# Performance work log

Measured on AMD Instinct MI355X. Metric: run time of the kernel, lower is better.

## Reference

```python
import jax, jax.numpy as jnp
import numpy as np

B, T, D = 32, 4096, 768
HEADS, DK, DV = 4, 64, 64
REL_W = 32
HIDDEN = 256


def setup_inputs() -> dict:
    key = jax.random.key(0)
    ks = jax.random.split(key, 12)
    H_sent = jax.random.normal(ks[0], (B, T, D), dtype=jnp.float32)
    # realistic padding: each sample has a random valid length in [2048, T]
    lengths = jax.random.randint(ks[1], (B,), 2048, T + 1)
    attention_mask_sent = (jnp.arange(T)[None, :] < lengths[:, None]).astype(jnp.int32)
    noun_pos = jax.random.randint(ks[2], (B,), 0, 2048).astype(jnp.int32)
    pooled_fields = jax.random.normal(ks[3], (B, D), dtype=jnp.float32)
    # xavier-uniform for (heads, d, dk): fan_in=d, fan_out=dk per torch semantics
    def xavier(k, shape, fan_in, fan_out):
        lim = float(np.sqrt(6.0 / (fan_in + fan_out)))
        return jax.random.uniform(k, shape, jnp.float32, -lim, lim)
    WQ = xavier(ks[4], (HEADS, D, DK), D, DK)
    WK = xavier(ks[5], (HEADS, D, DK), D, DK)
    WV = xavier(ks[6], (HEADS, D, DV), D, DV)
    rel_bias = jnp.zeros((HEADS, 2 * REL_W + 1), jnp.float32) + 0.01 * jax.random.normal(ks[7], (HEADS, 2 * REL_W + 1))
    in_proj = D + HEADS * DV + D  # 1792
    proj_w = xavier(ks[8], (HIDDEN, in_proj), in_proj, HIDDEN)
    proj_b = jnp.zeros((HIDDEN,), jnp.float32)
    mlp_w = xavier(ks[9], (2, HIDDEN), HIDDEN, 2)
    mlp_b = jnp.zeros((2,), jnp.float32)
    return {
        "H_sent": H_sent, "attention_mask_sent": attention_mask_sent,
        "noun_pos": noun_pos, "pooled_fields": pooled_fields,
        "WQ": WQ, "WK": WK, "WV": WV, "rel_bias": rel_bias,
        "proj_w": proj_w, "proj_b": proj_b, "mlp_w": mlp_w, "mlp_b": mlp_b,
    }


def reference(H_sent, attention_mask_sent, noun_pos, pooled_fields,
              WQ, WK, WV, rel_bias, proj_w, proj_b, mlp_w, mlp_b):
    b, t, d = H_sent.shape
    heads, _, dk = WQ.shape
    w = (rel_bias.shape[1] - 1) // 2
    # gather single query vector per sample
    h_i = H_sent[jnp.arange(b), noun_pos]  # (B, d)
    Q = jnp.einsum('bd,hdk->bhk', h_i, WQ)        # (B, H, dk)
    K = jnp.einsum('btd,hdk->bthk', H_sent, WK)   # (B, T, H, dk)
    V = jnp.einsum('btd,hdv->bthv', H_sent, WV)   # (B, T, H, dv)
    scores = jnp.einsum('bhk,bthk->bht', Q, K) / jnp.sqrt(jnp.float32(dk))  # (B,H,T)
    # relative-position bias gathered by clamped delta
    delta = jnp.clip(jnp.arange(t)[None, :] - noun_pos[:, None], -w, w) + w  # (B,T)
    rb = rel_bias[:, delta]                        # (H, B, T)
    scores = scores + jnp.transpose(rb, (1, 0, 2))
    scores = jnp.where(attention_mask_sent[:, None, :] == 0, jnp.float32(-1e9), scores)
    alpha = jax.nn.softmax(scores, axis=-1)        # (B, H, T)
    c = jnp.einsum('bht,bthv->bhv', alpha, V).reshape(b, -1)  # (B, H*dv)
    r = jnp.concatenate([h_i, c, pooled_fields], axis=-1)     # (B, d + H*dv + d)
    hdn = jax.nn.gelu(r @ proj_w.T + proj_b, approximate=False)
    logits = hdn @ mlp_w.T + mlp_b                 # (B, 2)
    return logits
```

## Files before the change

### kernel.cpp

```cpp
#include <hip/hip_runtime.h>
#include <math.h>

#define BB 32
#define TT 4096
#define DD 768
#define NH 4
#define RELW 32
#define NREL 65
#define HIDDEN 256
#define INPROJ 1792

#define NCH 32
#define CROWS (TT / NCH)
#define TROWS 8
#define C4 (DD / 4)

#define WAITVM6() asm volatile("s_waitcnt vmcnt(6)" ::: "memory")
#define WAITVM0() asm volatile("s_waitcnt vmcnt(0)" ::: "memory")

__device__ __forceinline__ void gl_lds16(const float* g, float* l) {
    __builtin_amdgcn_global_load_lds(
        (const __attribute__((address_space(1))) float*)(uintptr_t)g,
        (__attribute__((address_space(3))) float*)(uintptr_t)l,
        16, 0, 0);
}

template <int CTRL, int RMASK>
__device__ __forceinline__ float upd0(float x) {
    return __int_as_float(__builtin_amdgcn_update_dpp(
        0, __float_as_int(x), CTRL, RMASK, 0xf, true));
}
__device__ __forceinline__ float wave_sum64(float x) {
    x += upd0<0x111, 0xf>(x);
    x += upd0<0x112, 0xf>(x);
    x += upd0<0x114, 0xf>(x);
    x += upd0<0x118, 0xf>(x);
    x += upd0<0x142, 0xa>(x);
    x += upd0<0x143, 0xc>(x);
    return __int_as_float(__builtin_amdgcn_readlane(__float_as_int(x), 63));
}

__global__ __launch_bounds__(256) void kA(const float* __restrict__ H,
                                          const int* __restrict__ noun_pos,
                                          const float* __restrict__ WQ,
                                          const float* __restrict__ WK,
                                          float* __restrict__ R,
                                          float* __restrict__ qk_ws) {
    int b = blockIdx.x / NH, h = blockIdx.x % NH;
    __shared__ float hi_s[DD];
    __shared__ float q_s[64];
    int tn = noun_pos[b];
    const float* Hrow = H + ((size_t)b * TT + tn) * DD;
    for (int d = threadIdx.x; d < DD; d += 256) {
        float v = Hrow[d];
        hi_s[d] = v;
        if (h == 0) R[(size_t)b * INPROJ + d] = v;
    }
    __syncthreads();
    if (threadIdx.x < 64) {
        int k = threadIdx.x;
        const float* wq = WQ + (size_t)h * DD * 64 + k;
        float acc = 0.f;
        for (int d = 0; d < DD; ++d) acc += hi_s[d] * wq[(size_t)d * 64];
        q_s[k] = acc;
    }
    __syncthreads();
    for (int d = threadIdx.x; d < DD; d += 256) {
        const float* wk = WK + ((size_t)h * DD + d) * 64;
        float acc = 0.f;
        #pragma unroll
        for (int k = 0; k < 64; ++k) acc += q_s[k] * wk[k];
        qk_ws[((size_t)b * NH + h) * DD + d] = acc * 0.125f;
    }
}

#define DOT(ACC, CV, QV) ACC += CV.x*QV.x + CV.y*QV.y + CV.z*QV.z + CV.w*QV.w

#define HUPD(M, L, S0, S1, B0, B1, B2)                                    \
  {                                                                        \
    float nm = fmaxf(M, fmaxf(S0, S1));                                    \
    if (nm > M + 8.0f) {                                                   \
      float sc = __expf(M - nm);                                           \
      L *= sc;                                                             \
      B0.x*=sc; B0.y*=sc; B0.z*=sc; B0.w*=sc;                              \
      B1.x*=sc; B1.y*=sc; B1.z*=sc; B1.w*=sc;                              \
      B2.x*=sc; B2.y*=sc; B2.z*=sc; B2.w*=sc;                              \
      M = nm;                                                              \
    }                                                                      \
    float p0 = __expf(S0 - M), p1 = __expf(S1 - M);                        \
    L += p0 + p1;                                                          \
    B0.x += p0*c0.x + p1*c3.x; B0.y += p0*c0.y + p1*c3.y;                  \
    B0.z += p0*c0.z + p1*c3.z; B0.w += p0*c0.w + p1*c3.w;                  \
    B1.x += p0*c1.x + p1*c4.x; B1.y += p0*c1.y + p1*c4.y;                  \
    B1.z += p0*c1.z + p1*c4.z; B1.w += p0*c1.w + p1*c4.w;                  \
    B2.x += p0*c2.x + p1*c5.x; B2.y += p0*c2.y + p1*c5.y;                  \
    B2.z += p0*c2.z + p1*c5.z; B2.w += p0*c2.w + p1*c5.w;                  \
  }

__global__ __launch_bounds__(256, 3) void kFlash(const float* __restrict__ H,
                                                 const int* __restrict__ mask,
                                                 const int* __restrict__ noun_pos,
                                                 const float* __restrict__ rel_bias,
                                                 const float* __restrict__ qk_ws,
                                                 float* __restrict__ macc,
                                                 float* __restrict__ ml) {
    const int b   = blockIdx.x / NCH;
    const int ch  = blockIdx.x % NCH;
    const int tid = threadIdx.x;
    const int wave = tid >> 6, lane = tid & 63;

    __shared__ float4 Hts[2][TROWS * C4];
    __shared__ float4 rbL[CROWS];
    __shared__ float mls[4][8];
    __shared__ int snl;

    const int t0 = ch * CROWS;
    const int tn = noun_pos[b];

    if (tid == 0) snl = 0;
    __syncthreads();
    if (tid < CROWS) {
        int t = t0 + tid;
        int dl = t - tn; dl = dl < -RELW ? -RELW : (dl > RELW ? RELW : dl);
        int mm = mask[(size_t)b * TT + t];
        float4 rv;
        if (mm) {
            rv.x = rel_bias[0 * NREL + dl + RELW];
            rv.y = rel_bias[1 * NREL + dl + RELW];
            rv.z = rel_bias[2 * NREL + dl + RELW];
            rv.w = rel_bias[3 * NREL + dl + RELW];
            atomicMax(&snl, tid + 1);
        } else {
            rv.x = rv.y = rv.z = rv.w = -2.0e9f;
        }
        rbL[tid] = rv;
    }

    float4 qr[NH][3];
    {
        const float4* qk4 = (const float4*)(qk_ws + (size_t)b * NH * DD);
        #pragma unroll
        for (int h = 0; h < NH; ++h)
            #pragma unroll
            for (int j = 0; j < 3; ++j)
                qr[h][j] = qk4[h * C4 + j * 64 + lane];
    }

    __syncthreads();
    const int NTE = (snl + TROWS - 1) / TROWS;

    if (NTE == 0) {
        float4 z = {0.f, 0.f, 0.f, 0.f};
        float4* mo = (float4*)(macc + (size_t)blockIdx.x * NH * DD);
        int h = tid >> 6, ln = tid & 63;
        #pragma unroll
        for (int j = 0; j < 3; ++j) mo[h * C4 + j * 64 + ln] = z;
        if (tid < NH) {
            float* mp = ml + (size_t)blockIdx.x * NH * 2;
            mp[tid * 2 + 0] = -3.0e38f; mp[tid * 2 + 1] = 0.f;
        }
        return;
    }

    float m0 = -3.0e38f, m1 = -3.0e38f, m2 = -3.0e38f, m3 = -3.0e38f;
    float l0 = 0.f, l1 = 0.f, l2 = 0.f, l3 = 0.f;
    float4 A00{0,0,0,0}, A01{0,0,0,0}, A02{0,0,0,0};
    float4 A10{0,0,0,0}, A11{0,0,0,0}, A12{0,0,0,0};
    float4 A20{0,0,0,0}, A21{0,0,0,0}, A22{0,0,0,0};
    float4 A30{0,0,0,0}, A31{0,0,0,0}, A32{0,0,0,0};

    const float* Hc = H + ((size_t)b * TT + t0) * DD;
    const int woff = wave * 1536;

    {
        float* dst = (float*)&Hts[0][0] + woff;
        const float* src = Hc + woff;
        #pragma unroll
        for (int i = 0; i < 6; ++i)
            gl_lds16(src + i * 256 + lane * 4, dst + i * 256);
    }

    #pragma unroll 1
    for (int t = 0; t < NTE; ++t) {
        const int cur = t & 1;
        if (t + 1 < NTE) {
            float* dst = (float*)&Hts[cur ^ 1][0] + woff;
            const float* src = Hc + (size_t)(t + 1) * TROWS * DD + woff;
            #pragma unroll
            for (int i = 0; i < 6; ++i)
                gl_lds16(src + i * 256 + lane * 4, dst + i * 256);
            WAITVM6();
        } else {
            WAITVM0();
        }
        const float4* Hr = &Hts[cur][0] + wave * 384;
        float4 c0 = Hr[lane],       c1 = Hr[64 + lane],  c2 = Hr[128 + lane];
        float4 c3 = Hr[192 + lane], c4 = Hr[256 + lane], c5 = Hr[320 + lane];

        float s00 = 0, s01 = 0, s02 = 0, s03 = 0;
        float s10 = 0, s11 = 0, s12 = 0, s13 = 0;
        DOT(s00, c0, qr[0][0]); DOT(s00, c1, qr[0][1]); DOT(s00, c2, qr[0][2]);
        DOT(s01, c0, qr[1][0]); DOT(s01, c1, qr[1][1]); DOT(s01, c2, qr[1][2]);
        DOT(s02, c0, qr[2][0]); DOT(s02, c1, qr[2][1]); DOT(s02, c2, qr[2][2]);
        DOT(s03, c0, qr[3][0]); DOT(s03, c1, qr[3][1]); DOT(s03, c2, qr[3][2]);
        DOT(s10, c3, qr[0][0]); DOT(s10, c4, qr[0][1]); DOT(s10, c5, qr[0][2]);
        DOT(s11, c3, qr[1][0]); DOT(s11, c4, qr[1][1]); DOT(s11, c5, qr[1][2]);
        DOT(s12, c3, qr[2][0]); DOT(s12, c4, qr[2][1]); DOT(s12, c5, qr[2][2]);
        DOT(s13, c3, qr[3][0]); DOT(s13, c4, qr[3][1]); DOT(s13, c5, qr[3][2]);
        float r00 = wave_sum64(s00), r01 = wave_sum64(s01);
        float r02 = wave_sum64(s02), r03 = wave_sum64(s03);
        float r10 = wave_sum64(s10), r11 = wave_sum64(s11);
        float r12 = wave_sum64(s12), r13 = wave_sum64(s13);
        float4 rb0 = rbL[t * TROWS + 2 * wave];
        float4 rb1 = rbL[t * TROWS + 2 * wave + 1];
        r00 += rb0.x; r01 += rb0.y; r02 += rb0.z; r03 += rb0.w;
        r10 += rb1.x; r11 += rb1.y; r12 += rb1.z; r13 += rb1.w;
        HUPD(m0, l0, r00, r10, A00, A01, A02);
        HUPD(m1, l1, r01, r11, A10, A11, A12);
        HUPD(m2, l2, r02, r12, A20, A21, A22);
        HUPD(m3, l3, r03, r13, A30, A31, A32);
    }

    __syncthreads();
    float4* scr = &Hts[0][0];
    #pragma unroll
    for (int j = 0; j < 3; ++j) {
        scr[(wave * 4 + 0) * C4 + j * 64 + lane] = j == 0 ? A00 : (j == 1 ? A01 : A02);
        scr[(wave * 4 + 1) * C4 + j * 64 + lane] = j == 0 ? A10 : (j == 1 ? A11 : A12);
        scr[(wave * 4 + 2) * C4 + j * 64 + lane] = j == 0 ? A20 : (j == 1 ? A21 : A22);
        scr[(wave * 4 + 3) * C4 + j * 64 + lane] = j == 0 ? A30 : (j == 1 ? A31 : A32);
    }
    if (lane == 0) {
        mls[wave][0] = m0; mls[wave][1] = l0; mls[wave][2] = m1; mls[wave][3] = l1;
        mls[wave][4] = m2; mls[wave][5] = l2; mls[wave][6] = m3; mls[wave][7] = l3;
    }
    __syncthreads();
    {
        int h = tid >> 6, ln = tid & 63;
        float M = fmaxf(fmaxf(mls[0][h*2], mls[1][h*2]), fmaxf(mls[2][h*2], mls[3][h*2]));
        float w0 = __expf(mls[0][h*2] - M), w1 = __expf(mls[1][h*2] - M);
        float w2 = __expf(mls[2][h*2] - M), w3 = __expf(mls[3][h*2] - M);
        float4* mo = (float4*)(macc + (size_t)blockIdx.x * NH * DD);
        #pragma unroll
        for (int j = 0; j < 3; ++j) {
            float4 v0 = scr[(0*4 + h) * C4 + j * 64 + ln];
            float4 v1 = scr[(1*4 + h) * C4 + j * 64 + ln];
            float4 v2 = scr[(2*4 + h) * C4 + j * 64 + ln];
            float4 v3 = scr[(3*4 + h) * C4 + j * 64 + ln];
            float4 v;
            v.x = w0*v0.x + w1*v1.x + w2*v2.x + w3*v3.x;
            v.y = w0*v0.y + w1*v1.y + w2*v2.y + w3*v3.y;
            v.z = w0*v0.z + w1*v1.z + w2*v2.z + w3*v3.z;
            v.w = w0*v0.w + w1*v1.w + w2*v2.w + w3*v3.w;
            mo[h * C4 + j * 64 + ln] = v;
        }
        if (tid < NH) {
            int hh = tid;
            float Mh = fmaxf(fmaxf(mls[0][hh*2], mls[1][hh*2]), fmaxf(mls[2][hh*2], mls[3][hh*2]));
            float Lh = __expf(mls[0][hh*2] - Mh) * mls[0][hh*2+1]
                     + __expf(mls[1][hh*2] - Mh) * mls[1][hh*2+1]
                     + __expf(mls[2][hh*2] - Mh) * mls[2][hh*2+1]
                     + __expf(mls[3][hh*2] - Mh) * mls[3][hh*2+1];
            float* mp = ml + (size_t)blockIdx.x * NH * 2;
            mp[hh * 2 + 0] = Mh; mp[hh * 2 + 1] = Lh;
        }
    }
}

__global__ __launch_bounds__(256) void kT(const float* __restrict__ pw,
                                          float* __restrict__ pwT) {
    int o = blockIdx.x * 256 + threadIdx.x;
    int j = o / INPROJ, i = o % INPROJ;
    pwT[(size_t)i * HIDDEN + j] = pw[o];
}

__global__ __launch_bounds__(256) void kComb(const float* __restrict__ macc,
                                             const float* __restrict__ ml,
                                             float* __restrict__ hbar) {
    int blk = blockIdx.x;
    int b = blk / 12, rem = blk % 12, h = rem / 3, dseg = rem % 3;
    int d = dseg * 256 + threadIdx.x;
    const float* mlb = ml + (size_t)b * NCH * 8 + h * 2;
    float M = -3.0e38f;
    #pragma unroll 8
    for (int c = 0; c < NCH; ++c) M = fmaxf(M, mlb[(size_t)c * 8]);
    float L = 0.f;
    #pragma unroll 8
    for (int c = 0; c < NCH; ++c)
        L += __expf(mlb[(size_t)c * 8] - M) * mlb[(size_t)c * 8 + 1];
    float acc = 0.f;
    const float* mc = macc + ((size_t)b * NCH * NH + h) * DD + d;
    #pragma unroll 8
    for (int c = 0; c < NCH; ++c)
        acc += __expf(mlb[(size_t)c * 8] - M) * mc[(size_t)c * NH * DD];
    hbar[((size_t)b * NH + h) * DD + d] = acc / L;
}

__global__ __launch_bounds__(256) void kC2(const float* __restrict__ hbar,
                                           const float* __restrict__ WV,
                                           const float* __restrict__ pooled,
                                           float* __restrict__ R) {
    int b = blockIdx.x;
    int h = threadIdx.x >> 6, v = threadIdx.x & 63;
    const float* hb = hbar + ((size_t)b * NH + h) * DD;
    const float* wv = WV + (size_t)h * DD * 64 + v;
    float acc = 0.f;
    #pragma unroll 8
    for (int d = 0; d < DD; ++d) acc += hb[d] * wv[(size_t)d * 64];
    R[(size_t)b * INPROJ + DD + threadIdx.x] = acc;
    for (int i = threadIdx.x; i < DD; i += 256)
        R[(size_t)b * INPROJ + DD + 256 + i] = pooled[(size_t)b * DD + i];
}

__global__ __launch_bounds__(256) void kH1(const float* __restrict__ R,
                                           const float* __restrict__ pwT,
                                           float* __restrict__ part2) {
    int b = blockIdx.x / 7, seg = blockIdx.x % 7;
    int j = threadIdx.x;
    __shared__ float r_s[256];
    r_s[j] = R[(size_t)b * INPROJ + seg * 256 + j];
    __syncthreads();
    float acc = 0.f;
    const float* pT = pwT + (size_t)seg * 256 * HIDDEN + j;
    #pragma unroll 8
    for (int i = 0; i < 256; ++i) acc += r_s[i] * pT[(size_t)i * HIDDEN];
    part2[((size_t)b * 7 + seg) * HIDDEN + j] = acc;
}

__global__ __launch_bounds__(256) void kH2(const float* __restrict__ part2,
                                           const float* __restrict__ pb,
                                           const float* __restrict__ mw,
                                           const float* __restrict__ mb,
                                           float* __restrict__ out) {
    int b = blockIdx.x, j = threadIdx.x;
    float acc = pb[j];
    #pragma unroll
    for (int s = 0; s < 7; ++s) acc += part2[((size_t)b * 7 + s) * HIDDEN + j];
    float hdn = 0.5f * acc * (1.f + erff(acc * 0.70710678118654752f));
    float p0 = hdn * mw[j];
    float p1 = hdn * mw[HIDDEN + j];
    #pragma unroll
    for (int off = 32; off; off >>= 1) {
        p0 += __shfl_xor(p0, off);
        p1 += __shfl_xor(p1, off);
    }
    __shared__ float r0[4], r1[4];
    if ((j & 63) == 0) {
        r0[j >> 6] = p0;
        r1[j >> 6] = p1;
    }
    __syncthreads();
    if (j == 0) {
        out[b * 2 + 0] = r0[0] + r0[1] + r0[2] + r0[3] + mb[0];
        out[b * 2 + 1] = r1[0] + r1[1] + r1[2] + r1[3] + mb[1];
    }
}

extern "C" void kernel_launch(void* const* d_in, const int* in_sizes, int n_in,
                              void* d_out, int out_size, void* d_ws, size_t ws_size,
                              hipStream_t stream) {
    const float* H      = (const float*)d_in[0];
    const int*   mask   = (const int*)d_in[1];
    const int*   noun   = (const int*)d_in[2];
    const float* pooled = (const float*)d_in[3];
    const float* WQ     = (const float*)d_in[4];
    const float* WK     = (const float*)d_in[5];
    const float* WV     = (const float*)d_in[6];
    const float* relb   = (const float*)d_in[7];
    const float* pw     = (const float*)d_in[8];
    const float* pb     = (const float*)d_in[9];
    const float* mw     = (const float*)d_in[10];
    const float* mb     = (const float*)d_in[11];
    float* out = (float*)d_out;

    float* ws    = (float*)d_ws;
    float* R     = ws;
    float* qk    = R + (size_t)BB * INPROJ;
    float* macc  = qk + (size_t)BB * NH * DD;
    float* ml    = macc + (size_t)BB * NCH * NH * DD;
    float* hbar  = ml + (size_t)BB * NCH * NH * 2;
    float* pwT   = hbar + (size_t)BB * NH * DD;
    float* part2 = pwT + (size_t)INPROJ * HIDDEN;

    kA<<<BB * NH, 256, 0, stream>>>(H, noun, WQ, WK, R, qk);
    kT<<<(HIDDEN * INPROJ) / 256, 256, 0, stream>>>(pw, pwT);
    kFlash<<<BB * NCH, 256, 0, stream>>>(H, mask, noun, relb, qk, macc, ml);
    kComb<<<BB * 12, 256, 0, stream>>>(macc, ml, hbar);
    kC2<<<BB, 256, 0, stream>>>(hbar, WV, pooled, R);
    kH1<<<BB * 7, 256, 0, stream>>>(R, pwT, part2);
    kH2<<<BB, 256, 0, stream>>>(part2, pb, mw, mb, out);
}
```

Before: 152.6 us.

## Fuse split-softmax combine with V projection and merge head MLP kernels

Merges the chunk-combine and value-projection kernels into one per-(batch, head) block that keeps the combined hidden vector in shared memory, and folds the two head-MLP kernels into one block per sample that runs the full 1792-long dot product. The pooled-field copy moves into the first kernel, and the Q projection there is spread across all 256 threads with a shared-memory partial reduction. The goal is fewer launches and fewer global round trips for intermediates. In exchange the head kernel runs only 32 blocks with a long serial loop, which may lower parallelism.

Result: no change. 154.3 us (+1.1%).

```diff
diff --git a/kernel.cpp b/kernel.cpp
--- a/kernel.cpp
+++ b/kernel.cpp
@@ -44,10 +44,12 @@
                                           const int* __restrict__ noun_pos,
                                           const float* __restrict__ WQ,
                                           const float* __restrict__ WK,
+                                          const float* __restrict__ pooled,
                                           float* __restrict__ R,
                                           float* __restrict__ qk_ws) {
     int b = blockIdx.x / NH, h = blockIdx.x % NH;
     __shared__ float hi_s[DD];
+    __shared__ float qpart[4][64];
     __shared__ float q_s[64];
     int tn = noun_pos[b];
     const float* Hrow = H + ((size_t)b * TT + tn) * DD;
@@ -55,15 +57,21 @@
         float v = Hrow[d];
         hi_s[d] = v;
         if (h == 0) R[(size_t)b * INPROJ + d] = v;
-    }
-    __syncthreads();
-    if (threadIdx.x < 64) {
-        int k = threadIdx.x;
+        if (h == 1) R[(size_t)b * INPROJ + DD + NH * 64 + d] = pooled[(size_t)b * DD + d];
+    }
+    __syncthreads();
+    {
+        int k = threadIdx.x & 63, ds = threadIdx.x >> 6;
         const float* wq = WQ + (size_t)h * DD * 64 + k;
         float acc = 0.f;
-        for (int d = 0; d < DD; ++d) acc += hi_s[d] * wq[(size_t)d * 64];
-        q_s[k] = acc;
-    }
+        #pragma unroll 8
+        for (int d = ds * 192; d < ds * 192 + 192; ++d) acc += hi_s[d] * wq[(size_t)d * 64];
+        qpart[ds][k] = acc;
+    }
+    __syncthreads();
+    if (threadIdx.x < 64)
+        q_s[threadIdx.x] = qpart[0][threadIdx.x] + qpart[1][threadIdx.x]
+                         + qpart[2][threadIdx.x] + qpart[3][threadIdx.x];
     __syncthreads();
     for (int d = threadIdx.x; d < DD; d += 256) {
         const float* wk = WK + ((size_t)h * DD + d) * 64;
@@ -274,68 +282,71 @@
     pwT[(size_t)i * HIDDEN + j] = pw[o];
 }
 
-__global__ __launch_bounds__(256) void kComb(const float* __restrict__ macc,
-                                             const float* __restrict__ ml,
-                                             float* __restrict__ hbar) {
-    int blk = blockIdx.x;
-    int b = blk / 12, rem = blk % 12, h = rem / 3, dseg = rem % 3;
-    int d = dseg * 256 + threadIdx.x;
-    const float* mlb = ml + (size_t)b * NCH * 8 + h * 2;
+__global__ __launch_bounds__(256) void kCombC2(const float* __restrict__ macc,
+                                               const float* __restrict__ ml,
+                                               const float* __restrict__ WV,
+                                               float* __restrict__ R) {
+    int b = blockIdx.x / NH, h = blockIdx.x % NH;
+    __shared__ float hbar_s[DD];
+    __shared__ float mlv[NCH][2];
+    __shared__ float cpart[4][64];
+
+    if (threadIdx.x < NCH) {
+        const float* mp = ml + ((size_t)(b * NCH + threadIdx.x) * NH + h) * 2;
+        mlv[threadIdx.x][0] = mp[0];
+        mlv[threadIdx.x][1] = mp[1];
+    }
+    __syncthreads();
     float M = -3.0e38f;
-    #pragma unroll 8
-    for (int c = 0; c < NCH; ++c) M = fmaxf(M, mlb[(size_t)c * 8]);
+    #pragma unroll
+    for (int c = 0; c < NCH; ++c) M = fmaxf(M, mlv[c][0]);
     float L = 0.f;
-    #pragma unroll 8
-    for (int c = 0; c < NCH; ++c)
-        L += __expf(mlb[(size_t)c * 8] - M) * mlb[(size_t)c * 8 + 1];
-    float acc = 0.f;
-    const float* mc = macc + ((size_t)b * NCH * NH + h) * DD + d;
-    #pragma unroll 8
-    for (int c = 0; c < NCH; ++c)
-        acc += __expf(mlb[(size_t)c * 8] - M) * mc[(size_t)c * NH * DD];
-    hbar[((size_t)b * NH + h) * DD + d] = acc / L;
-}
-
-__global__ __launch_bounds__(256) void kC2(const float* __restrict__ hbar,
-                                           const float* __restrict__ WV,
-                                           const float* __restrict__ pooled,
-                                           float* __restrict__ R) {
-    int b = blockIdx.x;
-    int h = threadIdx.x >> 6, v = threadIdx.x & 63;
-    const float* hb = hbar + ((size_t)b * NH + h) * DD;
-    const float* wv = WV + (size_t)h * DD * 64 + v;
-    float acc = 0.f;
-    #pragma unroll 8
-    for (int d = 0; d < DD; ++d) acc += hb[d] * wv[(size_t)d * 64];
-    R[(size_t)b * INPROJ + DD + threadIdx.x] = acc;
-    for (int i = threadIdx.x; i < DD; i += 256)
-        R[(size_t)b * INPROJ + DD + 256 + i] = pooled[(size_t)b * DD + i];
-}
-
-__global__ __launch_bounds__(256) void kH1(const float* __restrict__ R,
-                                           const float* __restrict__ pwT,
-                                           float* __restrict__ part2) {
-    int b = blockIdx.x / 7, seg = blockIdx.x % 7;
-    int j = threadIdx.x;
-    __shared__ float r_s[256];
-    r_s[j] = R[(size_t)b * INPROJ + seg * 256 + j];
-    __syncthreads();
-    float acc = 0.f;
-    const float* pT = pwT + (size_t)seg * 256 * HIDDEN + j;
-    #pragma unroll 8
-    for (int i = 0; i < 256; ++i) acc += r_s[i] * pT[(size_t)i * HIDDEN];
-    part2[((size_t)b * 7 + seg) * HIDDEN + j] = acc;
-}
-
-__global__ __launch_bounds__(256) void kH2(const float* __restrict__ part2,
-                                           const float* __restrict__ pb,
-                                           const float* __restrict__ mw,
-                                           const float* __restrict__ mb,
-                                           float* __restrict__ out) {
+    #pragma unroll
+    for (int c = 0; c < NCH; ++c) L += __expf(mlv[c][0] - M) * mlv[c][1];
+    float invL = 1.f / L;
+
+    #pragma unroll
+    for (int j = 0; j < 3; ++j) {
+        int d = threadIdx.x + 256 * j;
+        float acc = 0.f;
+        const float* mc = macc + ((size_t)b * NCH * NH + h) * DD + d;
+        #pragma unroll 8
+        for (int c = 0; c < NCH; ++c)
+            acc += __expf(mlv[c][0] - M) * mc[(size_t)c * NH * DD];
+        hbar_s[d] = acc;
+    }
+    __syncthreads();
+
+    {
+        int v = threadIdx.x & 63, ds = threadIdx.x >> 6;
+        const float* wv = WV + (size_t)h * DD * 64 + v;
+        float acc = 0.f;
+        #pragma unroll 8
+        for (int d = ds * 192; d < ds * 192 + 192; ++d)
+            acc += hbar_s[d] * wv[(size_t)d * 64];
+        cpart[ds][v] = acc;
+    }
+    __syncthreads();
+    if (threadIdx.x < 64) {
+        float cv = (cpart[0][threadIdx.x] + cpart[1][threadIdx.x]
+                  + cpart[2][threadIdx.x] + cpart[3][threadIdx.x]) * invL;
+        R[(size_t)b * INPROJ + DD + h * 64 + threadIdx.x] = cv;
+    }
+}
+
+__global__ __launch_bounds__(256) void kH(const float* __restrict__ R,
+                                          const float* __restrict__ pwT,
+                                          const float* __restrict__ pb,
+                                          const float* __restrict__ mw,
+                                          const float* __restrict__ mb,
+                                          float* __restrict__ out) {
     int b = blockIdx.x, j = threadIdx.x;
+    __shared__ float r_s[INPROJ];
+    for (int i = j; i < INPROJ; i += 256) r_s[i] = R[(size_t)b * INPROJ + i];
+    __syncthreads();
     float acc = pb[j];
-    #pragma unroll
-    for (int s = 0; s < 7; ++s) acc += part2[((size_t)b * 7 + s) * HIDDEN + j];
+    #pragma unroll 16
+    for (int i = 0; i < INPROJ; ++i) acc += r_s[i] * pwT[(size_t)i * HIDDEN + j];
     float hdn = 0.5f * acc * (1.f + erff(acc * 0.70710678118654752f));
     float p0 = hdn * mw[j];
     float p1 = hdn * mw[HIDDEN + j];
@@ -378,15 +389,11 @@
     float* qk    = R + (size_t)BB * INPROJ;
     float* macc  = qk + (size_t)BB * NH * DD;
     float* ml    = macc + (size_t)BB * NCH * NH * DD;
-    float* hbar  = ml + (size_t)BB * NCH * NH * 2;
-    float* pwT   = hbar + (size_t)BB * NH * DD;
-    float* part2 = pwT + (size_t)INPROJ * HIDDEN;
-
-    kA<<<BB * NH, 256, 0, stream>>>(H, noun, WQ, WK, R, qk);
+    float* pwT   = ml + (size_t)BB * NCH * NH * 2;
+
+    kA<<<BB * NH, 256, 0, stream>>>(H, noun, WQ, WK, pooled, R, qk);
     kT<<<(HIDDEN * INPROJ) / 256, 256, 0, stream>>>(pw, pwT);
     kFlash<<<BB * NCH, 256, 0, stream>>>(H, mask, noun, relb, qk, macc, ml);
-    kComb<<<BB * 12, 256, 0, stream>>>(macc, ml, hbar);
-    kC2<<<BB, 256, 0, stream>>>(hbar, WV, pooled, R);
-    kH1<<<BB * 7, 256, 0, stream>>>(R, pwT, part2);
-    kH2<<<BB, 256, 0, stream>>>(part2, pb, mw, mb, out);
-}
+    kCombC2<<<BB * NH, 256, 0, stream>>>(macc, ml, WV, R);
+    kH<<<BB, 256, 0, stream>>>(R, pwT, pb, mw, mb, out);
+}
```
